# Kernel optimization log

Hardware: AMD Instinct MI355X
Metric: run time of the kernel (lower is better)

## Reference

```python
import jax, jax.numpy as jnp
import numpy as np

N_HEAD = 16
N_EMBD = 2048
B, S = 2, 2048


def setup_inputs() -> dict:
    key = jax.random.key(0)
    k1, k2, k3 = jax.random.split(key, 3)
    scale = 0.02
    return {
        "hidden_states": jax.random.normal(k1, (B, S, N_EMBD), dtype=jnp.float32),
        "attention_mask": jnp.ones((B, S), dtype=jnp.float32),
        "w_attn": jax.random.normal(k2, (N_EMBD, 3 * N_EMBD), dtype=jnp.float32) * scale,
        "b_attn": jnp.zeros((3 * N_EMBD,), dtype=jnp.float32),
        "w_proj": jax.random.normal(k3, (N_EMBD, N_EMBD), dtype=jnp.float32) * scale,
        "b_proj": jnp.zeros((N_EMBD,), dtype=jnp.float32),
    }


def reference(hidden_states, attention_mask, w_attn, b_attn, w_proj, b_proj):
    b, s, d = hidden_states.shape
    h = N_HEAD
    dh = d // h
    qkv = hidden_states @ w_attn + b_attn          # [b, s, 3d]
    q, k, v = jnp.split(qkv, 3, axis=-1)
    # [b, s, d] -> [b, h, s, dh]
    q = q.reshape(b, s, h, dh).transpose(0, 2, 1, 3)
    k = k.reshape(b, s, h, dh).transpose(0, 2, 1, 3)
    v = v.reshape(b, s, h, dh).transpose(0, 2, 1, 3)
    scores = jnp.einsum("bhqd,bhkd->bhqk", q, k) / jnp.sqrt(jnp.float32(dh))
    # padding mask: [b, s] -> additive bias [b, 1, 1, s]
    bias = (1.0 - attention_mask)[:, None, None, :] * -10000.0
    attn = jax.nn.softmax(scores + bias, axis=-1)   # dropout p=0 (eval)
    out = jnp.einsum("bhqk,bhkd->bhqd", attn, v)    # [b, h, s, dh]
    out = out.transpose(0, 2, 1, 3).reshape(b, s, d)
    return out @ w_proj + b_proj
```

## Files before the change

kernel.cpp:

```cpp
#include <hip/hip_runtime.h>
#include <stdint.h>

#define B_   2
#define S_   2048
#define D_   2048
#define NH_  16
#define DH_  128
#define N3_  6144

typedef unsigned short u16;
typedef __bf16 bf16x8 __attribute__((ext_vector_type(8)));
typedef float  f32x4  __attribute__((ext_vector_type(4)));

#define QSCALE   (0.08838834764831845f * 1.4426950408889634f)
#define BIASF    (-10000.0f * 1.4426950408889634f)

__device__ __forceinline__ u16 f2bf(float f) {
  union { float f; unsigned u; } v; v.f = f;
  unsigned u = v.u;
  return (u16)((u + 0x7FFFu + ((u >> 16) & 1u)) >> 16);
}

__device__ __forceinline__ float fast_exp2(float x) {
  float r;
  asm("v_exp_f32 %0, %1" : "=v"(r) : "v"(x));
  return r;
}

__device__ __forceinline__ unsigned cvtpk(float lo, float hi) {
  unsigned r;
  asm("v_cvt_pk_bf16_f32 %0, %1, %2" : "=v"(r) : "v"(lo), "v"(hi));
  return r;
}

#define GL2LDS(gsrc, ldst)                                                              \
  __builtin_amdgcn_global_load_lds((const __attribute__((address_space(1))) void*)(gsrc), \
      (__attribute__((address_space(3))) void*)(ldst), 16, 0, 0)

__device__ __forceinline__ int swz_id() {
  int id = blockIdx.y * gridDim.x + blockIdx.x;
  int cpx = (gridDim.x * gridDim.y) >> 3;
  return (id & 7) * cpx + (id >> 3);
}

__global__ void cvt_kernel(const float* __restrict__ in, u16* __restrict__ out, int n4) {
  int i = blockIdx.x * blockDim.x + threadIdx.x;
  int stride = gridDim.x * blockDim.x;
  for (; i < n4; i += stride) {
    float4 v = ((const float4*)in)[i];
    ushort4 o;
    o.x = f2bf(v.x); o.y = f2bf(v.y); o.z = f2bf(v.z); o.w = f2bf(v.w);
    ((ushort4*)out)[i] = o;
  }
}

__global__ void transpose_kernel(const float* __restrict__ in, u16* __restrict__ out,
                                 int K, int N) {
  __shared__ float tile[32][33];
  int tx = threadIdx.x, ty = threadIdx.y;
  int nx = blockIdx.x * 32, ky = blockIdx.y * 32;
#pragma unroll
  for (int j = 0; j < 32; j += 8)
    tile[ty + j][tx] = in[(size_t)(ky + ty + j) * N + nx + tx];
  __syncthreads();
#pragma unroll
  for (int j = 0; j < 32; j += 8)
    out[(size_t)(nx + ty + j) * K + ky + tx] = f2bf(tile[tx][ty + j]);
}


#define G8_AB(c, qm) (lds + (c) * 24576 + (qm) * 8192)
#define G8_BB(c)     (lds + (c) * 24576 + 16384)
#define VMCNT(n) asm volatile("s_waitcnt vmcnt(" #n ")" ::: "memory")
#define LGKM0                                            \
  do {                                                   \
    asm volatile("s_waitcnt lgkmcnt(0)" ::: "memory");   \
    __builtin_amdgcn_sched_barrier(0);                   \
  } while (0)
#define BAR __builtin_amdgcn_s_barrier()

template <int KD>
__device__ __forceinline__ void stage_ah(const u16* __restrict__ A, u16* lds,
                                         int k, int qm, int m0, int t) {
  int c = k & 1;
#pragma unroll
  for (int inst = 0; inst < 2; ++inst) {
    int idx = inst * 512 + t;
    int hr = idx >> 3, p = idx & 7, L = p ^ (hr & 7);
    int r = ((hr >> 5) << 6) + qm * 32 + (hr & 31);
    GL2LDS(A + (size_t)(m0 + r) * KD + k * 64 + L * 8,
           G8_AB(c, qm) + idx * 8);
  }
}

template <int KD>
__device__ __forceinline__ void stage_bh(const u16* __restrict__ BT, u16* lds,
                                         int k, int n0, int t) {
  int c = k & 1;
#pragma unroll
  for (int inst = 0; inst < 2; ++inst) {
    int idx = inst * 512 + t;
    int hn = idx >> 3, p = idx & 7, L = p ^ (hn & 7);
    GL2LDS(BT + (size_t)(n0 + hn) * KD + k * 64 + L * 8,
           G8_BB(c) + idx * 8);
  }
}

__device__ __forceinline__ void read_aq(const u16* lds, int c, int qm, int wr, int g,
                                        int lr, bf16x8 (&af)[2][2]) {
  const u16* base = G8_AB(c, qm);
#pragma unroll
  for (int i = 0; i < 2; ++i) {
    int hr = wr * 32 + i * 16 + lr;
#pragma unroll
    for (int kk = 0; kk < 2; ++kk) {
      int slot = ((kk << 2) | g) ^ (hr & 7);
      af[i][kk] = *reinterpret_cast<const bf16x8*>(base + hr * 64 + slot * 8);
    }
  }
}

__device__ __forceinline__ void read_b(const u16* lds, int c, int wc, int g, int lr,
                                       bf16x8 (&bf)[4][2]) {
  const u16* base = G8_BB(c);
#pragma unroll
  for (int nj = 0; nj < 4; ++nj) {
    int hn = wc * 64 + nj * 16 + lr;
#pragma unroll
    for (int kk = 0; kk < 2; ++kk) {
      int slot = ((kk << 2) | g) ^ (hn & 7);
      bf[nj][kk] = *reinterpret_cast<const bf16x8*>(base + hn * 64 + slot * 8);
    }
  }
}

template <int QM>
__device__ __forceinline__ void mfma_q(const bf16x8 (&af)[2][2], const bf16x8 (&bf)[4][2],
                                       f32x4 (&acc)[4][4]) {
  __builtin_amdgcn_s_setprio(1);
#pragma unroll
  for (int i = 0; i < 2; ++i)
#pragma unroll
    for (int nj = 0; nj < 4; ++nj)
#pragma unroll
      for (int kk = 0; kk < 2; ++kk)
        acc[QM * 2 + i][nj] = __builtin_amdgcn_mfma_f32_16x16x32_bf16(
            af[i][kk], bf[nj][kk], acc[QM * 2 + i][nj], 0, 0, 0);
  __builtin_amdgcn_s_setprio(0);
}

template <int KD>
__device__ __forceinline__ void gemm8_core(const u16* __restrict__ A,
                                           const u16* __restrict__ BT,
                                           int m0, int n0, u16* lds, f32x4 (&acc)[4][4]) {
  const int NT = KD / 64;
  const int NC = NT / 2;
  int t = threadIdx.x, wv = t >> 6, lane = t & 63;
  int g = lane >> 4, lr = lane & 15;
  int wr = wv >> 1, wc = wv & 1;
  bf16x8 af[2][2], bf[4][2];

  stage_ah<KD>(A, lds, 0, 0, m0, t);
  stage_ah<KD>(A, lds, 0, 1, m0, t);
  stage_bh<KD>(BT, lds, 0, n0, t);
  stage_ah<KD>(A, lds, 1, 0, m0, t);
  stage_ah<KD>(A, lds, 1, 1, m0, t);
  stage_bh<KD>(BT, lds, 1, n0, t);
  VMCNT(0);
  BAR;

  for (int j = 0; j + 1 < NC; ++j) {
    read_aq(lds, 0, 0, wr, g, lr, af);
    read_b(lds, 0, wc, g, lr, bf);
    if (j >= 1) stage_ah<KD>(A, lds, 2 * j + 1, 1, m0, t);
    VMCNT(6); BAR; LGKM0;
    mfma_q<0>(af, bf, acc);
    BAR;
    read_aq(lds, 0, 1, wr, g, lr, af);
    stage_ah<KD>(A, lds, 2 * j + 2, 0, m0, t);
    stage_bh<KD>(BT, lds, 2 * j + 2, n0, t);
    VMCNT(6); BAR; LGKM0;
    mfma_q<1>(af, bf, acc);
    BAR;
    read_aq(lds, 1, 0, wr, g, lr, af);
    read_b(lds, 1, wc, g, lr, bf);
    stage_ah<KD>(A, lds, 2 * j + 2, 1, m0, t);
    VMCNT(6); BAR; LGKM0;
    mfma_q<0>(af, bf, acc);
    BAR;
    read_aq(lds, 1, 1, wr, g, lr, af);
    if (2 * j + 3 < NT) {
      stage_ah<KD>(A, lds, 2 * j + 3, 0, m0, t);
      stage_bh<KD>(BT, lds, 2 * j + 3, n0, t);
    }
    VMCNT(6); BAR; LGKM0;
    mfma_q<1>(af, bf, acc);
    BAR;
  }

  stage_ah<KD>(A, lds, NT - 1, 1, m0, t);
  VMCNT(0);
  BAR;
  read_aq(lds, 0, 0, wr, g, lr, af);
  read_b(lds, 0, wc, g, lr, bf);
  mfma_q<0>(af, bf, acc);
  read_aq(lds, 0, 1, wr, g, lr, af);
  mfma_q<1>(af, bf, acc);
  read_aq(lds, 1, 0, wr, g, lr, af);
  read_b(lds, 1, wc, g, lr, bf);
  mfma_q<0>(af, bf, acc);
  read_aq(lds, 1, 1, wr, g, lr, af);
  mfma_q<1>(af, bf, acc);
}

__global__ __launch_bounds__(512, 1) void gemm_qkv_kernel(
    const u16* __restrict__ A, const u16* __restrict__ BT, const float* __restrict__ bias,
    u16* __restrict__ Qb, u16* __restrict__ Kb, u16* __restrict__ VTb) {
  __shared__ __attribute__((aligned(16))) u16 lds[49152];
  f32x4 acc[4][4] = {};
  int sw = swz_id();
  int n0 = (sw % gridDim.x) * 128, m0 = (sw / gridDim.x) * 256;
  gemm8_core<2048>(A, BT, m0, n0, lds, acc);
  int t = threadIdx.x, lane = t & 63, wv = t >> 6;
  int g = lane >> 4, lr = lane & 15;
  int wrB = (wv >> 1) * 64, wcB = (wv & 1) * 64;
#pragma unroll
  for (int mi = 0; mi < 4; ++mi) {
    int rowbase = m0 + wrB + mi * 16 + g * 4;
    int b = rowbase >> 11, s = rowbase & 2047;
#pragma unroll
    for (int nj = 0; nj < 4; ++nj) {
      int col = n0 + wcB + nj * 16 + lr;
      float bv = bias[col];
      int sec = col >> 11;
      int within = col & 2047;
      int h = within >> 7, d = within & 127;
      if (sec < 2) {
        float mult = (sec == 0) ? QSCALE : 1.0f;
        u16* dst = (sec == 0 ? Qb : Kb) + ((size_t)(b * NH_ + h) * S_ + s) * DH_ + d;
#pragma unroll
        for (int r = 0; r < 4; ++r) dst[(size_t)r * DH_] = f2bf((acc[mi][nj][r] + bv) * mult);
      } else {
        u16* dst = VTb + ((size_t)(b * NH_ + h) * DH_ + d) * S_ + s;
        ushort4 pk;
        pk.x = f2bf(acc[mi][nj][0] + bv); pk.y = f2bf(acc[mi][nj][1] + bv);
        pk.z = f2bf(acc[mi][nj][2] + bv); pk.w = f2bf(acc[mi][nj][3] + bv);
        *reinterpret_cast<ushort4*>(dst) = pk;
      }
    }
  }
}

__global__ __launch_bounds__(512, 1) void gemm_proj_kernel(
    const u16* __restrict__ A, const u16* __restrict__ BT, const float* __restrict__ bias,
    float* __restrict__ out) {
  __shared__ __attribute__((aligned(16))) u16 lds[49152];
  f32x4 acc[4][4] = {};
  int sw = swz_id();
  int n0 = (sw % gridDim.x) * 128, m0 = (sw / gridDim.x) * 256;
  gemm8_core<2048>(A, BT, m0, n0, lds, acc);
  int t = threadIdx.x, lane = t & 63, wv = t >> 6;
  int g = lane >> 4, lr = lane & 15;
  int wrB = (wv >> 1) * 64, wcB = (wv & 1) * 64;
#pragma unroll
  for (int mi = 0; mi < 4; ++mi) {
    int rowbase = m0 + wrB + mi * 16 + g * 4;
#pragma unroll
    for (int nj = 0; nj < 4; ++nj) {
      int col = n0 + wcB + nj * 16 + lr;
      float bv = bias[col];
      float* dst = out + (size_t)rowbase * D_ + col;
#pragma unroll
      for (int r = 0; r < 4; ++r) dst[(size_t)r * D_] = acc[mi][nj][r] + bv;
    }
  }
}

__global__ __launch_bounds__(256) void attn_kernel(
    const u16* __restrict__ Qb, const u16* __restrict__ Kb, const u16* __restrict__ VTb,
    const float* __restrict__ mask, u16* __restrict__ AO) {
  __shared__ __attribute__((aligned(16))) u16 Ks[2][64 * 128];
  __shared__ __attribute__((aligned(16))) u16 Vs[2][128 * 64];
  __shared__ float bias_lds[S_];

  int t = threadIdx.x, w = t >> 6, lane = t & 63;
  int g = lane >> 4, lr = lane & 15;
  int sw = swz_id();
  int qt = sw & 31, bh = sw >> 5;
  int b = bh >> 4;
  const u16* Qh = Qb + (size_t)bh * S_ * DH_;
  const u16* Kh = Kb + (size_t)bh * S_ * DH_;
  const u16* Vh = VTb + (size_t)bh * DH_ * S_;
  int q0 = qt * 64 + w * 16;

  for (int i = t; i < S_; i += 256)
    bias_lds[i] = (1.0f - mask[b * S_ + i]) * BIASF;

  bf16x8 bq[4];
#pragma unroll
  for (int kk = 0; kk < 4; ++kk)
    bq[kk] = *reinterpret_cast<const bf16x8*>(Qh + (size_t)(q0 + lr) * DH_ + kk * 32 + g * 8);

  f32x4 oacc[8] = {};
  float m_r = -1e30f, l_r = 0.f;

  __syncthreads();

#define STAGE_KV(buf, s0base)                                                    \
  {                                                                              \
    _Pragma("unroll")                                                            \
    for (int i = 0; i < 4; ++i) {                                                \
      int idx = i * 256 + t;                                                     \
      int row = idx >> 4, slot = idx & 15;                                       \
      GL2LDS(Kh + (size_t)((s0base) + row) * DH_ + ((slot ^ (row & 7)) * 8),     \
             &Ks[buf][idx * 8]);                                                 \
    }                                                                            \
    _Pragma("unroll")                                                            \
    for (int i = 0; i < 4; ++i) {                                                \
      int idx = i * 256 + t;                                                     \
      int row = idx >> 3, slot = idx & 7;                                        \
      GL2LDS(Vh + (size_t)row * S_ + (s0base) + ((slot ^ (row & 7)) * 8),        \
             &Vs[buf][idx * 8]);                                                 \
    }                                                                            \
  }

  STAGE_KV(0, 0);
  const int NT = S_ / 64;
  for (int it = 0; it < NT; ++it) {
    int cur = it & 1;
    if (it + 1 < NT) {
      STAGE_KV(cur ^ 1, (it + 1) * 64);
      asm volatile("s_waitcnt vmcnt(8)" ::: "memory");
    } else {
      asm volatile("s_waitcnt vmcnt(0)" ::: "memory");
    }
    __builtin_amdgcn_s_barrier();
    __builtin_amdgcn_sched_barrier(0);

    f32x4 sacc[4] = {};
    __builtin_amdgcn_s_setprio(1);
#pragma unroll
    for (int kk = 0; kk < 4; ++kk) {
#pragma unroll
      for (int n = 0; n < 4; ++n) {
        int row = lr + 16 * n;
        bf16x8 ak = *reinterpret_cast<const bf16x8*>(
            &Ks[cur][row * 128 + ((((kk << 2) | g) ^ (row & 7)) * 8)]);
        sacc[n] = __builtin_amdgcn_mfma_f32_16x16x32_bf16(ak, bq[kk], sacc[n], 0, 0, 0);
      }
    }
    __builtin_amdgcn_s_setprio(0);

    int s0 = it * 64;
    float sv[4][4];
    float mloc = -3e38f;
#pragma unroll
    for (int n = 0; n < 4; ++n) {
      float4 bb = *reinterpret_cast<const float4*>(&bias_lds[s0 + 16 * n + g * 4]);
      sv[n][0] = sacc[n][0] + bb.x; sv[n][1] = sacc[n][1] + bb.y;
      sv[n][2] = sacc[n][2] + bb.z; sv[n][3] = sacc[n][3] + bb.w;
      mloc = fmaxf(mloc, fmaxf(fmaxf(sv[n][0], sv[n][1]), fmaxf(sv[n][2], sv[n][3])));
    }
    float mx = fmaxf(mloc, __shfl_xor(mloc, 16));
    mx = fmaxf(mx, __shfl_xor(mx, 32));

    if (__any(mx - m_r > 8.f)) {
      float mnew = fmaxf(m_r, mx);
      float f = fast_exp2(m_r - mnew);
      m_r = mnew;
      l_r *= f;
#pragma unroll
      for (int no = 0; no < 8; ++no) oacc[no] *= f;
    }

    unsigned pku[4][2];
#pragma unroll
    for (int n = 0; n < 4; ++n) {
      float p0 = fast_exp2(sv[n][0] - m_r), p1 = fast_exp2(sv[n][1] - m_r);
      float p2 = fast_exp2(sv[n][2] - m_r), p3 = fast_exp2(sv[n][3] - m_r);
      l_r += (p0 + p1) + (p2 + p3);
      pku[n][0] = cvtpk(p0, p1);
      pku[n][1] = cvtpk(p2, p3);
    }

    int srcA = ((g & 1) << 5) + lr;
    int srcB = srcA + 16;
    bool hi = (g >> 1) != 0;
#pragma unroll
    for (int kk2 = 0; kk2 < 2; ++kk2) {
      unsigned a0 = __shfl(pku[2 * kk2][0], srcA), a1 = __shfl(pku[2 * kk2 + 1][0], srcA);
      unsigned b0 = __shfl(pku[2 * kk2][1], srcA), b1 = __shfl(pku[2 * kk2 + 1][1], srcA);
      unsigned c0 = __shfl(pku[2 * kk2][0], srcB), c1 = __shfl(pku[2 * kk2 + 1][0], srcB);
      unsigned d0 = __shfl(pku[2 * kk2][1], srcB), d1 = __shfl(pku[2 * kk2 + 1][1], srcB);
      union { uint4 u; bf16x8 v; } pa;
      pa.u.x = hi ? a1 : a0; pa.u.y = hi ? b1 : b0;
      pa.u.z = hi ? c1 : c0; pa.u.w = hi ? d1 : d0;
      __builtin_amdgcn_s_setprio(1);
#pragma unroll
      for (int no = 0; no < 8; ++no) {
        int d = lr + 16 * no;
        bf16x8 av = *reinterpret_cast<const bf16x8*>(
            &Vs[cur][d * 64 + ((((kk2 << 2) | g) ^ (d & 7)) * 8)]);
        oacc[no] = __builtin_amdgcn_mfma_f32_16x16x32_bf16(av, pa.v, oacc[no], 0, 0, 0);
      }
      __builtin_amdgcn_s_setprio(0);
    }
    __builtin_amdgcn_sched_barrier(0);
    __builtin_amdgcn_s_barrier();
  }
#undef STAGE_KV

  float s = l_r;
  s += __shfl_xor(s, 16);
  s += __shfl_xor(s, 32);
  float inv = 1.0f / s;
  int h = bh & 15;
  int q = q0 + lr;
  u16* dst = AO + ((size_t)(b * S_ + q)) * D_ + h * DH_ + g * 4;
#pragma unroll
  for (int no = 0; no < 8; ++no) {
    ushort4 pk4;
    pk4.x = f2bf(oacc[no][0] * inv); pk4.y = f2bf(oacc[no][1] * inv);
    pk4.z = f2bf(oacc[no][2] * inv); pk4.w = f2bf(oacc[no][3] * inv);
    *reinterpret_cast<ushort4*>(dst + 16 * no) = pk4;
  }
}

extern "C" void kernel_launch(void* const* d_in, const int* in_sizes, int n_in,
                              void* d_out, int out_size, void* d_ws, size_t ws_size,
                              hipStream_t stream) {
  const float* h_in   = (const float*)d_in[0];
  const float* mask   = (const float*)d_in[1];
  const float* w_attn = (const float*)d_in[2];
  const float* b_attn = (const float*)d_in[3];
  const float* w_proj = (const float*)d_in[4];
  const float* b_proj = (const float*)d_in[5];
  float* out = (float*)d_out;

  char* ws = (char*)d_ws;
  u16* Hb  = (u16*)(ws);
  u16* W1T = (u16*)(ws + 16777216);
  u16* W2T = (u16*)(ws + 41943040);
  u16* Qb  = (u16*)(ws + 50331648);
  u16* Kb  = (u16*)(ws + 67108864);
  u16* VTb = (u16*)(ws + 83886080);
  u16* AO  = Hb;

  cvt_kernel<<<2048, 256, 0, stream>>>(h_in, Hb, (B_ * S_ * D_) / 4);
  dim3 tb(32, 8);
  transpose_kernel<<<dim3(N3_ / 32, D_ / 32), tb, 0, stream>>>(w_attn, W1T, D_, N3_);
  transpose_kernel<<<dim3(D_ / 32, D_ / 32), tb, 0, stream>>>(w_proj, W2T, D_, D_);
  gemm_qkv_kernel<<<dim3(N3_ / 128, (B_ * S_) / 256), 512, 0, stream>>>(
      Hb, W1T, b_attn, Qb, Kb, VTb);
  attn_kernel<<<dim3(S_ / 64, B_ * NH_), 256, 0, stream>>>(Qb, Kb, VTb, mask, AO);
  gemm_proj_kernel<<<dim3(D_ / 128, (B_ * S_) / 256), 512, 0, stream>>>(AO, W2T, b_proj, out);
}
```

Measured before the change: 424.9 us.

## Process two 16-row query slices per wave in attention to reuse K/V LDS reads

Each attention wave now handles 32 query rows as two 16-row sub-tiles, so a block covers 128 queries and the grid is halved. Each K and V fragment loaded from LDS feeds two MFMAs instead of one, halving LDS traffic and global K/V staging per query. The cost is doubled accumulator registers (two sets of oacc, sacc, softmax state), a launch_bounds occupancy hint of 2, and fewer blocks (512) to fill the GPU. The swz_id mapping now uses 16 query tiles per head, which assumes the hidden swizzle helper matches the new grid.

```diff
diff --git a/kernel.cpp b/kernel.cpp
--- a/kernel.cpp
+++ b/kernel.cpp
@@ -67,7 +67,6 @@
   for (int j = 0; j < 32; j += 8)
     out[(size_t)(nx + ty + j) * K + ky + tx] = f2bf(tile[tx][ty + j]);
 }
-
 
 #define G8_AB(c, qm) (lds + (c) * 24576 + (qm) * 8192)
 #define G8_BB(c)     (lds + (c) * 24576 + 16384)
@@ -276,7 +275,7 @@
   }
 }
 
-__global__ __launch_bounds__(256) void attn_kernel(
+__global__ __launch_bounds__(256, 2) void attn_kernel(
     const u16* __restrict__ Qb, const u16* __restrict__ Kb, const u16* __restrict__ VTb,
     const float* __restrict__ mask, u16* __restrict__ AO) {
   __shared__ __attribute__((aligned(16))) u16 Ks[2][64 * 128];
@@ -286,23 +285,26 @@
   int t = threadIdx.x, w = t >> 6, lane = t & 63;
   int g = lane >> 4, lr = lane & 15;
   int sw = swz_id();
-  int qt = sw & 31, bh = sw >> 5;
+  int qt = sw & 15, bh = sw >> 4;
   int b = bh >> 4;
   const u16* Qh = Qb + (size_t)bh * S_ * DH_;
   const u16* Kh = Kb + (size_t)bh * S_ * DH_;
   const u16* Vh = VTb + (size_t)bh * DH_ * S_;
-  int q0 = qt * 64 + w * 16;
+  int q0 = qt * 128 + w * 32;
 
   for (int i = t; i < S_; i += 256)
     bias_lds[i] = (1.0f - mask[b * S_ + i]) * BIASF;
 
-  bf16x8 bq[4];
-#pragma unroll
-  for (int kk = 0; kk < 4; ++kk)
-    bq[kk] = *reinterpret_cast<const bf16x8*>(Qh + (size_t)(q0 + lr) * DH_ + kk * 32 + g * 8);
-
-  f32x4 oacc[8] = {};
-  float m_r = -1e30f, l_r = 0.f;
+  bf16x8 bq[2][4];
+#pragma unroll
+  for (int qs = 0; qs < 2; ++qs)
+#pragma unroll
+    for (int kk = 0; kk < 4; ++kk)
+      bq[qs][kk] = *reinterpret_cast<const bf16x8*>(
+          Qh + (size_t)(q0 + qs * 16 + lr) * DH_ + kk * 32 + g * 8);
+
+  f32x4 oacc[2][8] = {};
+  float m_r[2] = {-1e30f, -1e30f}, l_r[2] = {0.f, 0.f};
 
   __syncthreads();
 
@@ -337,7 +339,7 @@
     __builtin_amdgcn_s_barrier();
     __builtin_amdgcn_sched_barrier(0);
 
-    f32x4 sacc[4] = {};
+    f32x4 sacc[2][4] = {};
     __builtin_amdgcn_s_setprio(1);
 #pragma unroll
     for (int kk = 0; kk < 4; ++kk) {
@@ -346,41 +348,49 @@
         int row = lr + 16 * n;
         bf16x8 ak = *reinterpret_cast<const bf16x8*>(
             &Ks[cur][row * 128 + ((((kk << 2) | g) ^ (row & 7)) * 8)]);
-        sacc[n] = __builtin_amdgcn_mfma_f32_16x16x32_bf16(ak, bq[kk], sacc[n], 0, 0, 0);
+        sacc[0][n] = __builtin_amdgcn_mfma_f32_16x16x32_bf16(ak, bq[0][kk], sacc[0][n], 0, 0, 0);
+        sacc[1][n] = __builtin_amdgcn_mfma_f32_16x16x32_bf16(ak, bq[1][kk], sacc[1][n], 0, 0, 0);
       }
     }
     __builtin_amdgcn_s_setprio(0);
 
     int s0 = it * 64;
-    float sv[4][4];
-    float mloc = -3e38f;
-#pragma unroll
-    for (int n = 0; n < 4; ++n) {
-      float4 bb = *reinterpret_cast<const float4*>(&bias_lds[s0 + 16 * n + g * 4]);
-      sv[n][0] = sacc[n][0] + bb.x; sv[n][1] = sacc[n][1] + bb.y;
-      sv[n][2] = sacc[n][2] + bb.z; sv[n][3] = sacc[n][3] + bb.w;
-      mloc = fmaxf(mloc, fmaxf(fmaxf(sv[n][0], sv[n][1]), fmaxf(sv[n][2], sv[n][3])));
-    }
-    float mx = fmaxf(mloc, __shfl_xor(mloc, 16));
-    mx = fmaxf(mx, __shfl_xor(mx, 32));
-
-    if (__any(mx - m_r > 8.f)) {
-      float mnew = fmaxf(m_r, mx);
-      float f = fast_exp2(m_r - mnew);
-      m_r = mnew;
-      l_r *= f;
-#pragma unroll
-      for (int no = 0; no < 8; ++no) oacc[no] *= f;
-    }
-
-    unsigned pku[4][2];
-#pragma unroll
-    for (int n = 0; n < 4; ++n) {
-      float p0 = fast_exp2(sv[n][0] - m_r), p1 = fast_exp2(sv[n][1] - m_r);
-      float p2 = fast_exp2(sv[n][2] - m_r), p3 = fast_exp2(sv[n][3] - m_r);
-      l_r += (p0 + p1) + (p2 + p3);
-      pku[n][0] = cvtpk(p0, p1);
-      pku[n][1] = cvtpk(p2, p3);
+    float4 bb[4];
+#pragma unroll
+    for (int n = 0; n < 4; ++n)
+      bb[n] = *reinterpret_cast<const float4*>(&bias_lds[s0 + 16 * n + g * 4]);
+
+    unsigned pku[2][4][2];
+#pragma unroll
+    for (int qs = 0; qs < 2; ++qs) {
+      float sv[4][4];
+      float mloc = -3e38f;
+#pragma unroll
+      for (int n = 0; n < 4; ++n) {
+        sv[n][0] = sacc[qs][n][0] + bb[n].x; sv[n][1] = sacc[qs][n][1] + bb[n].y;
+        sv[n][2] = sacc[qs][n][2] + bb[n].z; sv[n][3] = sacc[qs][n][3] + bb[n].w;
+        mloc = fmaxf(mloc, fmaxf(fmaxf(sv[n][0], sv[n][1]), fmaxf(sv[n][2], sv[n][3])));
+      }
+      float mx = fmaxf(mloc, __shfl_xor(mloc, 16));
+      mx = fmaxf(mx, __shfl_xor(mx, 32));
+
+      if (__any(mx - m_r[qs] > 8.f)) {
+        float mnew = fmaxf(m_r[qs], mx);
+        float f = fast_exp2(m_r[qs] - mnew);
+        m_r[qs] = mnew;
+        l_r[qs] *= f;
+#pragma unroll
+        for (int no = 0; no < 8; ++no) oacc[qs][no] *= f;
+      }
+
+#pragma unroll
+      for (int n = 0; n < 4; ++n) {
+        float p0 = fast_exp2(sv[n][0] - m_r[qs]), p1 = fast_exp2(sv[n][1] - m_r[qs]);
+        float p2 = fast_exp2(sv[n][2] - m_r[qs]), p3 = fast_exp2(sv[n][3] - m_r[qs]);
+        l_r[qs] += (p0 + p1) + (p2 + p3);
+        pku[qs][n][0] = cvtpk(p0, p1);
+        pku[qs][n][1] = cvtpk(p2, p3);
+      }
     }
 
     int srcA = ((g & 1) << 5) + lr;
@@ -388,20 +398,24 @@
     bool hi = (g >> 1) != 0;
 #pragma unroll
     for (int kk2 = 0; kk2 < 2; ++kk2) {
-      unsigned a0 = __shfl(pku[2 * kk2][0], srcA), a1 = __shfl(pku[2 * kk2 + 1][0], srcA);
-      unsigned b0 = __shfl(pku[2 * kk2][1], srcA), b1 = __shfl(pku[2 * kk2 + 1][1], srcA);
-      unsigned c0 = __shfl(pku[2 * kk2][0], srcB), c1 = __shfl(pku[2 * kk2 + 1][0], srcB);
-      unsigned d0 = __shfl(pku[2 * kk2][1], srcB), d1 = __shfl(pku[2 * kk2 + 1][1], srcB);
-      union { uint4 u; bf16x8 v; } pa;
-      pa.u.x = hi ? a1 : a0; pa.u.y = hi ? b1 : b0;
-      pa.u.z = hi ? c1 : c0; pa.u.w = hi ? d1 : d0;
+      union { uint4 u; bf16x8 v; } pa[2];
+#pragma unroll
+      for (int qs = 0; qs < 2; ++qs) {
+        unsigned a0 = __shfl(pku[qs][2 * kk2][0], srcA), a1 = __shfl(pku[qs][2 * kk2 + 1][0], srcA);
+        unsigned b0 = __shfl(pku[qs][2 * kk2][1], srcA), b1 = __shfl(pku[qs][2 * kk2 + 1][1], srcA);
+        unsigned c0 = __shfl(pku[qs][2 * kk2][0], srcB), c1 = __shfl(pku[qs][2 * kk2 + 1][0], srcB);
+        unsigned d0 = __shfl(pku[qs][2 * kk2][1], srcB), d1 = __shfl(pku[qs][2 * kk2 + 1][1], srcB);
+        pa[qs].u.x = hi ? a1 : a0; pa[qs].u.y = hi ? b1 : b0;
+        pa[qs].u.z = hi ? c1 : c0; pa[qs].u.w = hi ? d1 : d0;
+      }
       __builtin_amdgcn_s_setprio(1);
 #pragma unroll
       for (int no = 0; no < 8; ++no) {
         int d = lr + 16 * no;
         bf16x8 av = *reinterpret_cast<const bf16x8*>(
             &Vs[cur][d * 64 + ((((kk2 << 2) | g) ^ (d & 7)) * 8)]);
-        oacc[no] = __builtin_amdgcn_mfma_f32_16x16x32_bf16(av, pa.v, oacc[no], 0, 0, 0);
+        oacc[0][no] = __builtin_amdgcn_mfma_f32_16x16x32_bf16(av, pa[0].v, oacc[0][no], 0, 0, 0);
+        oacc[1][no] = __builtin_amdgcn_mfma_f32_16x16x32_bf16(av, pa[1].v, oacc[1][no], 0, 0, 0);
       }
       __builtin_amdgcn_s_setprio(0);
     }
@@ -410,19 +424,22 @@
   }
 #undef STAGE_KV
 
-  float s = l_r;
-  s += __shfl_xor(s, 16);
-  s += __shfl_xor(s, 32);
-  float inv = 1.0f / s;
   int h = bh & 15;
-  int q = q0 + lr;
-  u16* dst = AO + ((size_t)(b * S_ + q)) * D_ + h * DH_ + g * 4;
-#pragma unroll
-  for (int no = 0; no < 8; ++no) {
-    ushort4 pk4;
-    pk4.x = f2bf(oacc[no][0] * inv); pk4.y = f2bf(oacc[no][1] * inv);
-    pk4.z = f2bf(oacc[no][2] * inv); pk4.w = f2bf(oacc[no][3] * inv);
-    *reinterpret_cast<ushort4*>(dst + 16 * no) = pk4;
+#pragma unroll
+  for (int qs = 0; qs < 2; ++qs) {
+    float s = l_r[qs];
+    s += __shfl_xor(s, 16);
+    s += __shfl_xor(s, 32);
+    float inv = 1.0f / s;
+    int q = q0 + qs * 16 + lr;
+    u16* dst = AO + ((size_t)(b * S_ + q)) * D_ + h * DH_ + g * 4;
+#pragma unroll
+    for (int no = 0; no < 8; ++no) {
+      ushort4 pk4;
+      pk4.x = f2bf(oacc[qs][no][0] * inv); pk4.y = f2bf(oacc[qs][no][1] * inv);
+      pk4.z = f2bf(oacc[qs][no][2] * inv); pk4.w = f2bf(oacc[qs][no][3] * inv);
+      *reinterpret_cast<ushort4*>(dst + 16 * no) = pk4;
+    }
   }
 }
 
@@ -452,6 +469,6 @@
   transpose_kernel<<<dim3(D_ / 32, D_ / 32), tb, 0, stream>>>(w_proj, W2T, D_, D_);
   gemm_qkv_kernel<<<dim3(N3_ / 128, (B_ * S_) / 256), 512, 0, stream>>>(
       Hb, W1T, b_attn, Qb, Kb, VTb);
-  attn_kernel<<<dim3(S_ / 64, B_ * NH_), 256, 0, stream>>>(Qb, Kb, VTb, mask, AO);
+  attn_kernel<<<dim3(S_ / 128, B_ * NH_), 256, 0, stream>>>(Qb, Kb, VTb, mask, AO);
   gemm_proj_kernel<<<dim3(D_ / 128, (B_ * S_) / 256), 512, 0, stream>>>(AO, W2T, b_proj, out);
 }
```

Result: faster. 400.5 us (-5.8%).
